# Kernel tuning notes

Hardware: AMD Instinct MI355X
Metric: run time of the kernel (lower is better)

The kernel has to match this reference:

```python
import jax, jax.numpy as jnp
import numpy as np

B, S, K, N, GROUPS, GS = 4, 2048, 4096, 4096, 32, 128


def setup_inputs() -> dict:
    key = jax.random.key(0)
    k1, k2, k3, k4, k5 = jax.random.split(key, 5)
    x = jax.random.normal(k1, (B, S, K), dtype=jnp.float32)
    # int8-stored quantized weights in [-128, 127], layout [K, N] (in_features, out_features)
    weight_int8 = jax.random.randint(k2, (K, N), -128, 128, dtype=jnp.int32)
    # per-group, per-output-column positive scales
    scales = (jax.random.uniform(k3, (GROUPS, N), dtype=jnp.float32) * 0.01 + 1e-4)
    bias = jax.random.normal(k4, (N,), dtype=jnp.float32) * 0.02
    # column reordering permutation (high-sensitivity cols first in the real module)
    col_indices = jax.random.permutation(k5, K).astype(jnp.int32)
    return {"x": x, "scales": scales, "bias": bias,
            "weight_int8": weight_int8, "col_indices": col_indices,
            "group_size": GS}


def reference(x, scales, bias, weight_int8, col_indices, group_size):
    orig_shape = x.shape
    k = x.shape[-1]
    x2 = x.reshape(-1, k)                      # [M, K]
    # CPR column reordering of the activations (weights are stored pre-reordered)
    x_reordered = x2[:, col_indices]           # [M, K]
    # per-group dequant: scale row-group g applies to rows [g*gs, (g+1)*gs) of W
    s_full = jnp.repeat(scales, group_size, axis=0)[:k]          # [K, N]
    w_deq = weight_int8.astype(x.dtype) * s_full                 # [K, N]
    y = x_reordered @ w_deq + bias                               # [M, N]
    return y.reshape(*orig_shape[:-1], y.shape[-1])
```

## Files before the change

kernel.cpp:

```cpp
#include <hip/hip_runtime.h>
#include <hip/hip_bf16.h>

#define M_DIM 8192
#define N_DIM 4096
#define K_DIM 4096
#define NITER 32

typedef __bf16 bf16x8 __attribute__((ext_vector_type(8)));
typedef float f32x4 __attribute__((ext_vector_type(4)));
typedef unsigned short ushort8v __attribute__((ext_vector_type(8)));

typedef const __attribute__((address_space(1))) void gv_t;
typedef __attribute__((address_space(3))) void lv_t;

static __device__ __forceinline__ unsigned short f2bf(float f) {
  unsigned u = __builtin_bit_cast(unsigned, f);
  u += 0x7fffu + ((u >> 16) & 1u);
  return (unsigned short)(u >> 16);
}

__global__ void k_pinv(const int* __restrict__ ci, int* __restrict__ pinv) {
  int k = blockIdx.x * 256 + threadIdx.x;
  if (k < K_DIM) pinv[ci[k]] = k;
}

__global__ void k_cvt(const float* __restrict__ x, unsigned short* __restrict__ xb) {
  const long n4 = (long)M_DIM * K_DIM / 4;
  for (long i = (long)blockIdx.x * 256 + threadIdx.x; i < n4; i += 2048L * 256) {
    float4 v = *(const float4*)(x + i * 4);
    ushort4 o;
    o.x = f2bf(v.x); o.y = f2bf(v.y); o.z = f2bf(v.z); o.w = f2bf(v.w);
    *(ushort4*)(xb + i * 4) = o;
  }
}

__global__ void k_w2t(const int* __restrict__ w, const float* __restrict__ scales,
                      const int* __restrict__ pinv, unsigned short* __restrict__ w2t) {
  __shared__ int tile[64 * 68];
  __shared__ int grp[64];
  __shared__ int krow[64];
  const int n0 = blockIdx.x * 64;
  const int c0 = blockIdx.y * 64;
  const int t = threadIdx.x;
  if (t < 64) {
    int kk = pinv[c0 + t];
    krow[t] = kk;
    grp[t] = kk >> 7;
  }
  __syncthreads();
  {
    const int ci = t >> 2, q = t & 3;
    const int kk = krow[ci];
    const int* src = w + (long)kk * N_DIM + n0 + q * 16;
#pragma unroll
    for (int j = 0; j < 4; ++j) {
      int4 v = *(const int4*)(src + j * 4);
      *(int4*)&tile[ci * 68 + q * 16 + j * 4] = v;
    }
  }
  __syncthreads();
  {
    const int nj = t >> 2, cq = t & 3;
    const int n = n0 + nj;
    unsigned short outv[16];
#pragma unroll
    for (int i = 0; i < 16; ++i) {
      int cii = cq * 16 + i;
      float f = (float)tile[cii * 68 + nj] * scales[grp[cii] * N_DIM + n];
      outv[i] = f2bf(f);
    }
    unsigned short* dst = w2t + (long)n * K_DIM + c0 + cq * 16;
    *(ushort8v*)(dst)     = *(ushort8v*)&outv[0];
    *(ushort8v*)(dst + 8) = *(ushort8v*)&outv[8];
  }
}

#define RD_A4(base) do { const char* _b=(const char*)(base); \
  af[0]=*(const bf16x8*)(_b); af[1]=*(const bf16x8*)(_b+2048); \
  af[2]=*(const bf16x8*)(_b+4096); af[3]=*(const bf16x8*)(_b+6144); } while(0)
#define RD_B4(base) do { const char* _b=(const char*)(base); \
  bf[0]=*(const bf16x8*)(_b); bf[1]=*(const bf16x8*)(_b+2048); \
  bf[2]=*(const bf16x8*)(_b+4096); bf[3]=*(const bf16x8*)(_b+6144); } while(0)
#define MFMA16(o) do { \
  _Pragma("unroll") for (int mi = 0; mi < 4; ++mi) \
  _Pragma("unroll") for (int ni = 0; ni < 4; ++ni) \
    acc[(o)+mi][ni] = __builtin_amdgcn_mfma_f32_16x16x32_bf16(af[mi], bf[ni], acc[(o)+mi][ni], 0, 0, 0); \
  } while(0)
#define GL(s, d) __builtin_amdgcn_global_load_lds((gv_t*)(s), (lv_t*)(d), 16, 0, 0)
#define BAR_IN() do { __builtin_amdgcn_s_barrier(); \
  asm volatile("s_waitcnt lgkmcnt(0)" ::: "memory"); \
  __builtin_amdgcn_sched_barrier(0); } while(0)
#define BAR_OUT() do { __builtin_amdgcn_sched_barrier(0); \
  __builtin_amdgcn_s_barrier(); __builtin_amdgcn_sched_barrier(0); } while(0)
#define VM4() asm volatile("s_waitcnt vmcnt(4)" ::: "memory")

__global__ __launch_bounds__(512, 2) void k_gemm(const unsigned short* __restrict__ A,
                                                 const unsigned short* __restrict__ Bt,
                                                 const float* __restrict__ bias,
                                                 float* __restrict__ C) {
  __shared__ __attribute__((aligned(16))) char lds[131072];
  char* A0 = lds;
  char* B0 = lds + 32768;
  char* A1 = lds + 65536;
  char* B1 = lds + 98304;

  const int bid = blockIdx.x;
  const int swz = (bid & 7) * 64 + (bid >> 3);
  const int by = swz >> 4;
  const int bx = swz & 15;

  const int tid = threadIdx.x;
  const int l = tid & 63;
  const int w = tid >> 6;
  const int wr = w >> 2;
  const int wc = w & 3;
  const int r4 = l & 15;
  const int kb = (l >> 4) << 4;

  const int wmask = ((tid >> 3) & 7) << 4;
  const int kbo = ((tid & 7) * 16) ^ wmask;
  const char* srcA = (const char*)A + (size_t)(by * 256 + (tid >> 3)) * (K_DIM * 2) + kbo;
  const char* srcB = (const char*)Bt + (size_t)(bx * 256 + (tid >> 3)) * (K_DIM * 2) + kbo;
  const int stgoff = tid * 16;

  const int R0A = wr * 128 + r4;
  const int R0B = wc * 64 + r4;
  const int aoff = ((R0A << 7) + kb) ^ ((R0A & 7) << 4);
  const int boff = ((R0B << 7) + kb) ^ ((R0B & 7) << 4);

  f32x4 acc[8][4];
  const f32x4 z = {0.f, 0.f, 0.f, 0.f};
#pragma unroll
  for (int mi = 0; mi < 8; ++mi)
#pragma unroll
    for (int ni = 0; ni < 4; ++ni) acc[mi][ni] = z;

#pragma unroll
  for (int j = 0; j < 4; ++j) GL(srcA + j * 524288, A0 + j * 8192 + stgoff);
#pragma unroll
  for (int j = 0; j < 4; ++j) GL(srcB + j * 524288, B0 + j * 8192 + stgoff);
#pragma unroll
  for (int j = 0; j < 2; ++j) GL(srcB + 128 + j * 524288, B1 + j * 8192 + stgoff);
  asm volatile("s_waitcnt vmcnt(2)" ::: "memory");
  BAR_OUT();

  bf16x8 af[4], bf[4];

  for (int J = 0; J < NITER; ++J) {
    const bool nl = (J < NITER - 1);
    const long ko1 = (long)(2 * J + 1) * 128;
    const long ko2 = ko1 + 128;
    const long ko3 = ko1 + 256;

    RD_A4(A0 + aoff);
    RD_B4(B0 + boff);
    GL(srcB + ko1 + 2 * 524288, B1 + 2 * 8192 + stgoff);
    GL(srcB + ko1 + 3 * 524288, B1 + 3 * 8192 + stgoff);
    BAR_IN();
    __builtin_amdgcn_s_setprio(1); MFMA16(0); __builtin_amdgcn_s_setprio(0);
    VM4();
    BAR_OUT();

    RD_A4(A0 + aoff + 8192);
    GL(srcA + ko1 + 0 * 524288, A1 + 0 * 8192 + stgoff);
    GL(srcA + ko1 + 2 * 524288, A1 + 2 * 8192 + stgoff);
    BAR_IN();
    __builtin_amdgcn_s_setprio(1); MFMA16(4); __builtin_amdgcn_s_setprio(0);
    BAR_OUT();

    RD_A4(A0 + (aoff ^ 64));
    RD_B4(B0 + (boff ^ 64));
    GL(srcA + ko1 + 1 * 524288, A1 + 1 * 8192 + stgoff);
    GL(srcA + ko1 + 3 * 524288, A1 + 3 * 8192 + stgoff);
    BAR_IN();
    __builtin_amdgcn_s_setprio(1); MFMA16(0); __builtin_amdgcn_s_setprio(0);
    BAR_OUT();

    RD_A4(A0 + (aoff ^ 64) + 8192);
    if (nl) {
      GL(srcB + ko2 + 0 * 524288, B0 + 0 * 8192 + stgoff);
      GL(srcB + ko2 + 1 * 524288, B0 + 1 * 8192 + stgoff);
    }
    BAR_IN();
    __builtin_amdgcn_s_setprio(1); MFMA16(4); __builtin_amdgcn_s_setprio(0);
    if (nl) VM4();
    else    asm volatile("s_waitcnt vmcnt(0)" ::: "memory");
    BAR_OUT();

    RD_A4(A1 + aoff);
    RD_B4(B1 + boff);
    if (nl) {
      GL(srcB + ko2 + 2 * 524288, B0 + 2 * 8192 + stgoff);
      GL(srcB + ko2 + 3 * 524288, B0 + 3 * 8192 + stgoff);
    }
    BAR_IN();
    __builtin_amdgcn_s_setprio(1); MFMA16(0); __builtin_amdgcn_s_setprio(0);
    VM4();
    BAR_OUT();

    RD_A4(A1 + aoff + 8192);
    if (nl) {
      GL(srcA + ko2 + 0 * 524288, A0 + 0 * 8192 + stgoff);
      GL(srcA + ko2 + 2 * 524288, A0 + 2 * 8192 + stgoff);
    }
    BAR_IN();
    __builtin_amdgcn_s_setprio(1); MFMA16(4); __builtin_amdgcn_s_setprio(0);
    BAR_OUT();

    RD_A4(A1 + (aoff ^ 64));
    RD_B4(B1 + (boff ^ 64));
    if (nl) {
      GL(srcA + ko2 + 1 * 524288, A0 + 1 * 8192 + stgoff);
      GL(srcA + ko2 + 3 * 524288, A0 + 3 * 8192 + stgoff);
    }
    BAR_IN();
    __builtin_amdgcn_s_setprio(1); MFMA16(0); __builtin_amdgcn_s_setprio(0);
    BAR_OUT();

    RD_A4(A1 + (aoff ^ 64) + 8192);
    if (nl) {
      GL(srcB + ko3 + 0 * 524288, B1 + 0 * 8192 + stgoff);
      GL(srcB + ko3 + 1 * 524288, B1 + 1 * 8192 + stgoff);
    }
    BAR_IN();
    __builtin_amdgcn_s_setprio(1); MFMA16(4); __builtin_amdgcn_s_setprio(0);
    VM4();
    BAR_OUT();
  }

  const int row0 = by * 256 + wr * 128 + ((l >> 4) << 2);
  const int col0 = bx * 256 + wc * 64 + r4;
#pragma unroll
  for (int ni = 0; ni < 4; ++ni) {
    const int col = col0 + ni * 16;
    const float bv = bias[col];
#pragma unroll
    for (int mi = 0; mi < 8; ++mi) {
#pragma unroll
      for (int r = 0; r < 4; ++r)
        C[(size_t)(row0 + mi * 16 + r) * N_DIM + col] = acc[mi][ni][r] + bv;
    }
  }
}

__global__ void k_fallback(const float* __restrict__ x, const float* __restrict__ scales,
                           const float* __restrict__ bias, const int* __restrict__ w,
                           const int* __restrict__ ci, float* __restrict__ out) {
  const int n = blockIdx.x * 256 + threadIdx.x;
  const int m0 = blockIdx.y * 32;
  float acc[32];
#pragma unroll
  for (int i = 0; i < 32; ++i) acc[i] = 0.f;
  for (int k = 0; k < K_DIM; ++k) {
    int c = ci[k];
    float wv = (float)w[(long)k * N_DIM + n] * scales[(k >> 7) * N_DIM + n];
#pragma unroll 8
    for (int mm = 0; mm < 32; ++mm)
      acc[mm] += x[(long)(m0 + mm) * K_DIM + c] * wv;
  }
  float bv = bias[n];
  for (int mm = 0; mm < 32; ++mm)
    out[(long)(m0 + mm) * N_DIM + n] = acc[mm] + bv;
}

extern "C" void kernel_launch(void* const* d_in, const int* in_sizes, int n_in,
                              void* d_out, int out_size, void* d_ws, size_t ws_size,
                              hipStream_t stream) {
  const float* x      = (const float*)d_in[0];
  const float* scales = (const float*)d_in[1];
  const float* bias   = (const float*)d_in[2];
  const int*   wq     = (const int*)d_in[3];
  const int*   ci     = (const int*)d_in[4];
  float* out = (float*)d_out;

  const size_t xb_bytes  = (size_t)M_DIM * K_DIM * 2;
  const size_t w2t_bytes = (size_t)N_DIM * K_DIM * 2;
  const size_t need = xb_bytes + w2t_bytes + (size_t)K_DIM * 4;

  if (ws_size < need) {
    k_fallback<<<dim3(N_DIM / 256, M_DIM / 32), 256, 0, stream>>>(x, scales, bias, wq, ci, out);
    return;
  }

  unsigned short* xb  = (unsigned short*)d_ws;
  unsigned short* w2t = (unsigned short*)((char*)d_ws + xb_bytes);
  int* pinv           = (int*)((char*)d_ws + xb_bytes + w2t_bytes);

  k_pinv<<<K_DIM / 256, 256, 0, stream>>>(ci, pinv);
  k_cvt<<<2048, 256, 0, stream>>>(x, xb);
  k_w2t<<<dim3(N_DIM / 64, K_DIM / 64), 256, 0, stream>>>(wq, scales, pinv, w2t);
  k_gemm<<<(M_DIM / 256) * (N_DIM / 256), 512, 0, stream>>>(xb, w2t, bias, out);
}
```

Measured before the change: 298.8 us.

## Switch GEMM inner loop from 16x16x32 to 32x32x16 bf16 MFMA tiles

Replaces the per-wave 8x4 grid of 16x16x32 MFMAs with a 4x2 grid of 32x32x16 MFMAs over the same 128x64 warp tile. LDS read addressing, the swizzle and the output epilogue row mapping are reworked to match the 32x32 accumulator layout. The intent is fewer MFMA issues and fewer LDS fragment reads per flop. The vmcnt waits are also renumbered to fit the new load count. The risk is accumulator register pressure and new LDS bank-conflict patterns from the changed swizzle.

New measurement: 323.5 us. 1.08x slower.

```diff
diff --git a/kernel.cpp b/kernel.cpp
--- a/kernel.cpp
+++ b/kernel.cpp
@@ -7,7 +7,7 @@
 #define NITER 32
 
 typedef __bf16 bf16x8 __attribute__((ext_vector_type(8)));
-typedef float f32x4 __attribute__((ext_vector_type(4)));
+typedef float f32x16 __attribute__((ext_vector_type(16)));
 typedef unsigned short ushort8v __attribute__((ext_vector_type(8)));
 
 typedef const __attribute__((address_space(1))) void gv_t;
@@ -75,16 +75,25 @@
   }
 }
 
-#define RD_A4(base) do { const char* _b=(const char*)(base); \
-  af[0]=*(const bf16x8*)(_b); af[1]=*(const bf16x8*)(_b+2048); \
-  af[2]=*(const bf16x8*)(_b+4096); af[3]=*(const bf16x8*)(_b+6144); } while(0)
-#define RD_B4(base) do { const char* _b=(const char*)(base); \
-  bf[0]=*(const bf16x8*)(_b); bf[1]=*(const bf16x8*)(_b+2048); \
-  bf[2]=*(const bf16x8*)(_b+4096); bf[3]=*(const bf16x8*)(_b+6144); } while(0)
-#define MFMA16(o) do { \
-  _Pragma("unroll") for (int mi = 0; mi < 4; ++mi) \
-  _Pragma("unroll") for (int ni = 0; ni < 4; ++ni) \
-    acc[(o)+mi][ni] = __builtin_amdgcn_mfma_f32_16x16x32_bf16(af[mi], bf[ni], acc[(o)+mi][ni], 0, 0, 0); \
+#define RDA(mh, bo, jp) do { \
+  af[0][0]=*(const bf16x8*)(lds+(bo)+(vA0^(((2*(jp))    )<<5))+((mh)*2+0)*4096); \
+  af[0][1]=*(const bf16x8*)(lds+(bo)+(vA0^(((2*(jp))+1  )<<5))+((mh)*2+0)*4096); \
+  af[1][0]=*(const bf16x8*)(lds+(bo)+(vA0^(((2*(jp))    )<<5))+((mh)*2+1)*4096); \
+  af[1][1]=*(const bf16x8*)(lds+(bo)+(vA0^(((2*(jp))+1  )<<5))+((mh)*2+1)*4096); } while(0)
+#define RDB(bo, jp) do { \
+  bf[0][0]=*(const bf16x8*)(lds+(bo)+32768+(vB0^(((2*(jp))  )<<5))      ); \
+  bf[0][1]=*(const bf16x8*)(lds+(bo)+32768+(vB0^(((2*(jp))+1)<<5))      ); \
+  bf[1][0]=*(const bf16x8*)(lds+(bo)+32768+(vB0^(((2*(jp))  )<<5))+4096 ); \
+  bf[1][1]=*(const bf16x8*)(lds+(bo)+32768+(vB0^(((2*(jp))+1)<<5))+4096 ); } while(0)
+#define MFMA8(mh) do { \
+  acc[(mh)*2+0][0]=__builtin_amdgcn_mfma_f32_32x32x16_bf16(af[0][0],bf[0][0],acc[(mh)*2+0][0],0,0,0); \
+  acc[(mh)*2+0][1]=__builtin_amdgcn_mfma_f32_32x32x16_bf16(af[0][0],bf[1][0],acc[(mh)*2+0][1],0,0,0); \
+  acc[(mh)*2+1][0]=__builtin_amdgcn_mfma_f32_32x32x16_bf16(af[1][0],bf[0][0],acc[(mh)*2+1][0],0,0,0); \
+  acc[(mh)*2+1][1]=__builtin_amdgcn_mfma_f32_32x32x16_bf16(af[1][0],bf[1][0],acc[(mh)*2+1][1],0,0,0); \
+  acc[(mh)*2+0][0]=__builtin_amdgcn_mfma_f32_32x32x16_bf16(af[0][1],bf[0][1],acc[(mh)*2+0][0],0,0,0); \
+  acc[(mh)*2+0][1]=__builtin_amdgcn_mfma_f32_32x32x16_bf16(af[0][1],bf[1][1],acc[(mh)*2+0][1],0,0,0); \
+  acc[(mh)*2+1][0]=__builtin_amdgcn_mfma_f32_32x32x16_bf16(af[1][1],bf[0][1],acc[(mh)*2+1][0],0,0,0); \
+  acc[(mh)*2+1][1]=__builtin_amdgcn_mfma_f32_32x32x16_bf16(af[1][1],bf[1][1],acc[(mh)*2+1][1],0,0,0); \
   } while(0)
 #define GL(s, d) __builtin_amdgcn_global_load_lds((gv_t*)(s), (lv_t*)(d), 16, 0, 0)
 #define BAR_IN() do { __builtin_amdgcn_s_barrier(); \
@@ -92,17 +101,12 @@
   __builtin_amdgcn_sched_barrier(0); } while(0)
 #define BAR_OUT() do { __builtin_amdgcn_sched_barrier(0); \
   __builtin_amdgcn_s_barrier(); __builtin_amdgcn_sched_barrier(0); } while(0)
-#define VM4() asm volatile("s_waitcnt vmcnt(4)" ::: "memory")
 
 __global__ __launch_bounds__(512, 2) void k_gemm(const unsigned short* __restrict__ A,
                                                  const unsigned short* __restrict__ Bt,
                                                  const float* __restrict__ bias,
                                                  float* __restrict__ C) {
   __shared__ __attribute__((aligned(16))) char lds[131072];
-  char* A0 = lds;
-  char* B0 = lds + 32768;
-  char* A1 = lds + 65536;
-  char* B1 = lds + 98304;
 
   const int bid = blockIdx.x;
   const int swz = (bid & 7) * 64 + (bid >> 3);
@@ -114,8 +118,6 @@
   const int w = tid >> 6;
   const int wr = w >> 2;
   const int wc = w & 3;
-  const int r4 = l & 15;
-  const int kb = (l >> 4) << 4;
 
   const int wmask = ((tid >> 3) & 7) << 4;
   const int kbo = ((tid & 7) * 16) ^ wmask;
@@ -123,28 +125,32 @@
   const char* srcB = (const char*)Bt + (size_t)(bx * 256 + (tid >> 3)) * (K_DIM * 2) + kbo;
   const int stgoff = tid * 16;
 
-  const int R0A = wr * 128 + r4;
-  const int R0B = wc * 64 + r4;
-  const int aoff = ((R0A << 7) + kb) ^ ((R0A & 7) << 4);
-  const int boff = ((R0B << 7) + kb) ^ ((R0B & 7) << 4);
-
-  f32x4 acc[8][4];
-  const f32x4 z = {0.f, 0.f, 0.f, 0.f};
-#pragma unroll
-  for (int mi = 0; mi < 8; ++mi)
-#pragma unroll
-    for (int ni = 0; ni < 4; ++ni) acc[mi][ni] = z;
-
-#pragma unroll
-  for (int j = 0; j < 4; ++j) GL(srcA + j * 524288, A0 + j * 8192 + stgoff);
-#pragma unroll
-  for (int j = 0; j < 4; ++j) GL(srcB + j * 524288, B0 + j * 8192 + stgoff);
-#pragma unroll
-  for (int j = 0; j < 2; ++j) GL(srcB + 128 + j * 524288, B1 + j * 8192 + stgoff);
+  const int lane31 = l & 31;
+  const int klo = (l >> 5) << 4;
+  const int rA = wr * 128 + lane31;
+  const int rB = wc * 64 + lane31;
+  const int mk = (l & 7) << 4;
+  const int vA0 = ((rA << 7) | klo) ^ mk;
+  const int vB0 = ((rB << 7) | klo) ^ mk;
+
+  f32x16 acc[4][2];
+#pragma unroll
+  for (int mi = 0; mi < 4; ++mi)
+#pragma unroll
+    for (int ni = 0; ni < 2; ++ni)
+#pragma unroll
+      for (int r = 0; r < 16; ++r) acc[mi][ni][r] = 0.f;
+
+#pragma unroll
+  for (int j = 0; j < 4; ++j) GL(srcA + j * 524288, lds + j * 8192 + stgoff);
+#pragma unroll
+  for (int j = 0; j < 4; ++j) GL(srcB + j * 524288, lds + 32768 + j * 8192 + stgoff);
+#pragma unroll
+  for (int j = 0; j < 2; ++j) GL(srcB + 128 + j * 524288, lds + 98304 + j * 8192 + stgoff);
   asm volatile("s_waitcnt vmcnt(2)" ::: "memory");
   BAR_OUT();
 
-  bf16x8 af[4], bf[4];
+  bf16x8 af[2][2], bf[2][2];
 
   for (int J = 0; J < NITER; ++J) {
     const bool nl = (J < NITER - 1);
@@ -152,93 +158,89 @@
     const long ko2 = ko1 + 128;
     const long ko3 = ko1 + 256;
 
-    RD_A4(A0 + aoff);
-    RD_B4(B0 + boff);
-    GL(srcB + ko1 + 2 * 524288, B1 + 2 * 8192 + stgoff);
-    GL(srcB + ko1 + 3 * 524288, B1 + 3 * 8192 + stgoff);
-    BAR_IN();
-    __builtin_amdgcn_s_setprio(1); MFMA16(0); __builtin_amdgcn_s_setprio(0);
-    VM4();
-    BAR_OUT();
-
-    RD_A4(A0 + aoff + 8192);
-    GL(srcA + ko1 + 0 * 524288, A1 + 0 * 8192 + stgoff);
-    GL(srcA + ko1 + 2 * 524288, A1 + 2 * 8192 + stgoff);
-    BAR_IN();
-    __builtin_amdgcn_s_setprio(1); MFMA16(4); __builtin_amdgcn_s_setprio(0);
-    BAR_OUT();
-
-    RD_A4(A0 + (aoff ^ 64));
-    RD_B4(B0 + (boff ^ 64));
-    GL(srcA + ko1 + 1 * 524288, A1 + 1 * 8192 + stgoff);
-    GL(srcA + ko1 + 3 * 524288, A1 + 3 * 8192 + stgoff);
-    BAR_IN();
-    __builtin_amdgcn_s_setprio(1); MFMA16(0); __builtin_amdgcn_s_setprio(0);
-    BAR_OUT();
-
-    RD_A4(A0 + (aoff ^ 64) + 8192);
-    if (nl) {
-      GL(srcB + ko2 + 0 * 524288, B0 + 0 * 8192 + stgoff);
-      GL(srcB + ko2 + 1 * 524288, B0 + 1 * 8192 + stgoff);
-    }
-    BAR_IN();
-    __builtin_amdgcn_s_setprio(1); MFMA16(4); __builtin_amdgcn_s_setprio(0);
-    if (nl) VM4();
+    RDA(0, 0, 0); RDB(0, 0);
+    GL(srcB + ko1 + 2 * 524288, lds + 98304 + 2 * 8192 + stgoff);
+    GL(srcB + ko1 + 3 * 524288, lds + 98304 + 3 * 8192 + stgoff);
+    BAR_IN();
+    __builtin_amdgcn_s_setprio(1); MFMA8(0); __builtin_amdgcn_s_setprio(0);
+    BAR_OUT();
+
+    RDA(1, 0, 0);
+    GL(srcA + ko1 + 0 * 524288, lds + 65536 + 0 * 8192 + stgoff);
+    GL(srcA + ko1 + 2 * 524288, lds + 65536 + 2 * 8192 + stgoff);
+    BAR_IN();
+    __builtin_amdgcn_s_setprio(1); MFMA8(1); __builtin_amdgcn_s_setprio(0);
+    BAR_OUT();
+
+    RDA(0, 0, 1); RDB(0, 1);
+    GL(srcA + ko1 + 1 * 524288, lds + 65536 + 1 * 8192 + stgoff);
+    GL(srcA + ko1 + 3 * 524288, lds + 65536 + 3 * 8192 + stgoff);
+    BAR_IN();
+    __builtin_amdgcn_s_setprio(1); MFMA8(0); __builtin_amdgcn_s_setprio(0);
+    BAR_OUT();
+
+    RDA(1, 0, 1);
+    if (nl) {
+      GL(srcB + ko2 + 0 * 524288, lds + 32768 + 0 * 8192 + stgoff);
+      GL(srcB + ko2 + 1 * 524288, lds + 32768 + 1 * 8192 + stgoff);
+    }
+    BAR_IN();
+    __builtin_amdgcn_s_setprio(1); MFMA8(1); __builtin_amdgcn_s_setprio(0);
+    if (nl) asm volatile("s_waitcnt vmcnt(2)" ::: "memory");
     else    asm volatile("s_waitcnt vmcnt(0)" ::: "memory");
     BAR_OUT();
 
-    RD_A4(A1 + aoff);
-    RD_B4(B1 + boff);
-    if (nl) {
-      GL(srcB + ko2 + 2 * 524288, B0 + 2 * 8192 + stgoff);
-      GL(srcB + ko2 + 3 * 524288, B0 + 3 * 8192 + stgoff);
-    }
-    BAR_IN();
-    __builtin_amdgcn_s_setprio(1); MFMA16(0); __builtin_amdgcn_s_setprio(0);
-    VM4();
-    BAR_OUT();
-
-    RD_A4(A1 + aoff + 8192);
-    if (nl) {
-      GL(srcA + ko2 + 0 * 524288, A0 + 0 * 8192 + stgoff);
-      GL(srcA + ko2 + 2 * 524288, A0 + 2 * 8192 + stgoff);
-    }
-    BAR_IN();
-    __builtin_amdgcn_s_setprio(1); MFMA16(4); __builtin_amdgcn_s_setprio(0);
-    BAR_OUT();
-
-    RD_A4(A1 + (aoff ^ 64));
-    RD_B4(B1 + (boff ^ 64));
-    if (nl) {
-      GL(srcA + ko2 + 1 * 524288, A0 + 1 * 8192 + stgoff);
-      GL(srcA + ko2 + 3 * 524288, A0 + 3 * 8192 + stgoff);
-    }
-    BAR_IN();
-    __builtin_amdgcn_s_setprio(1); MFMA16(0); __builtin_amdgcn_s_setprio(0);
-    BAR_OUT();
-
-    RD_A4(A1 + (aoff ^ 64) + 8192);
-    if (nl) {
-      GL(srcB + ko3 + 0 * 524288, B1 + 0 * 8192 + stgoff);
-      GL(srcB + ko3 + 1 * 524288, B1 + 1 * 8192 + stgoff);
-    }
-    BAR_IN();
-    __builtin_amdgcn_s_setprio(1); MFMA16(4); __builtin_amdgcn_s_setprio(0);
-    VM4();
-    BAR_OUT();
-  }
-
-  const int row0 = by * 256 + wr * 128 + ((l >> 4) << 2);
-  const int col0 = bx * 256 + wc * 64 + r4;
-#pragma unroll
-  for (int ni = 0; ni < 4; ++ni) {
-    const int col = col0 + ni * 16;
+    RDA(0, 65536, 0); RDB(65536, 0);
+    if (nl) {
+      GL(srcB + ko2 + 2 * 524288, lds + 32768 + 2 * 8192 + stgoff);
+      GL(srcB + ko2 + 3 * 524288, lds + 32768 + 3 * 8192 + stgoff);
+    }
+    BAR_IN();
+    __builtin_amdgcn_s_setprio(1); MFMA8(0); __builtin_amdgcn_s_setprio(0);
+    BAR_OUT();
+
+    RDA(1, 65536, 0);
+    if (nl) {
+      GL(srcA + ko2 + 0 * 524288, lds + 0 * 8192 + stgoff);
+      GL(srcA + ko2 + 2 * 524288, lds + 2 * 8192 + stgoff);
+    }
+    BAR_IN();
+    __builtin_amdgcn_s_setprio(1); MFMA8(1); __builtin_amdgcn_s_setprio(0);
+    BAR_OUT();
+
+    RDA(0, 65536, 1); RDB(65536, 1);
+    if (nl) {
+      GL(srcA + ko2 + 1 * 524288, lds + 1 * 8192 + stgoff);
+      GL(srcA + ko2 + 3 * 524288, lds + 3 * 8192 + stgoff);
+    }
+    BAR_IN();
+    __builtin_amdgcn_s_setprio(1); MFMA8(0); __builtin_amdgcn_s_setprio(0);
+    BAR_OUT();
+
+    RDA(1, 65536, 1);
+    if (nl) {
+      GL(srcB + ko3 + 0 * 524288, lds + 98304 + 0 * 8192 + stgoff);
+      GL(srcB + ko3 + 1 * 524288, lds + 98304 + 1 * 8192 + stgoff);
+    }
+    BAR_IN();
+    __builtin_amdgcn_s_setprio(1); MFMA8(1); __builtin_amdgcn_s_setprio(0);
+    asm volatile("s_waitcnt vmcnt(2)" ::: "memory");
+    BAR_OUT();
+  }
+
+  const int row0 = by * 256 + wr * 128 + ((l >> 5) << 2);
+  const int col0 = bx * 256 + wc * 64 + lane31;
+#pragma unroll
+  for (int ni = 0; ni < 2; ++ni) {
+    const int col = col0 + ni * 32;
     const float bv = bias[col];
 #pragma unroll
-    for (int mi = 0; mi < 8; ++mi) {
-#pragma unroll
-      for (int r = 0; r < 4; ++r)
-        C[(size_t)(row0 + mi * 16 + r) * N_DIM + col] = acc[mi][ni][r] + bv;
+    for (int mi = 0; mi < 4; ++mi) {
+#pragma unroll
+      for (int r = 0; r < 16; ++r) {
+        const int row = row0 + mi * 32 + (r & 3) + ((r >> 2) << 3);
+        C[(size_t)row * N_DIM + col] = acc[mi][ni][r] + bv;
+      }
     }
   }
 }
```

## Double-buffer MFMA fragments in registers and overlap LDS reads with compute

Applied to the files above, without the earlier changes.

Splits the A/B fragment registers into even/odd sets so the LDS reads for the next MFMA phase are issued before the current phase's MFMAs. Each phase then waits only on partial lgkmcnt (4 or 8 outstanding) instead of draining all LDS reads. The vmcnt waits are restructured from VM4 to VM2 at different points. This hides LDS latency behind matrix math, at the cost of extra VGPRs under the 512x2 launch bound and more delicate wait-count correctness.

Result: no change. 303.4 us (+1.5%).

```diff
diff --git a/kernel.cpp b/kernel.cpp
--- a/kernel.cpp
+++ b/kernel.cpp
@@ -75,24 +75,28 @@
   }
 }
 
-#define RD_A4(base) do { const char* _b=(const char*)(base); \
-  af[0]=*(const bf16x8*)(_b); af[1]=*(const bf16x8*)(_b+2048); \
-  af[2]=*(const bf16x8*)(_b+4096); af[3]=*(const bf16x8*)(_b+6144); } while(0)
-#define RD_B4(base) do { const char* _b=(const char*)(base); \
-  bf[0]=*(const bf16x8*)(_b); bf[1]=*(const bf16x8*)(_b+2048); \
-  bf[2]=*(const bf16x8*)(_b+4096); bf[3]=*(const bf16x8*)(_b+6144); } while(0)
-#define MFMA16(o) do { \
+#define RD4(dst, base) do { const char* _b=(const char*)(base); \
+  dst[0]=*(const bf16x8*)(_b); dst[1]=*(const bf16x8*)(_b+2048); \
+  dst[2]=*(const bf16x8*)(_b+4096); dst[3]=*(const bf16x8*)(_b+6144); } while(0)
+#define MFMA16(AF, BF, o) do { \
   _Pragma("unroll") for (int mi = 0; mi < 4; ++mi) \
   _Pragma("unroll") for (int ni = 0; ni < 4; ++ni) \
-    acc[(o)+mi][ni] = __builtin_amdgcn_mfma_f32_16x16x32_bf16(af[mi], bf[ni], acc[(o)+mi][ni], 0, 0, 0); \
+    acc[(o)+mi][ni] = __builtin_amdgcn_mfma_f32_16x16x32_bf16(AF[mi], BF[ni], acc[(o)+mi][ni], 0, 0, 0); \
   } while(0)
 #define GL(s, d) __builtin_amdgcn_global_load_lds((gv_t*)(s), (lv_t*)(d), 16, 0, 0)
-#define BAR_IN() do { __builtin_amdgcn_s_barrier(); \
+#define BAR_L0() do { __builtin_amdgcn_s_barrier(); \
   asm volatile("s_waitcnt lgkmcnt(0)" ::: "memory"); \
+  __builtin_amdgcn_sched_barrier(0); } while(0)
+#define BAR_L4() do { __builtin_amdgcn_s_barrier(); \
+  asm volatile("s_waitcnt lgkmcnt(4)" ::: "memory"); \
+  __builtin_amdgcn_sched_barrier(0); } while(0)
+#define BAR_L8() do { __builtin_amdgcn_s_barrier(); \
+  asm volatile("s_waitcnt lgkmcnt(8)" ::: "memory"); \
   __builtin_amdgcn_sched_barrier(0); } while(0)
 #define BAR_OUT() do { __builtin_amdgcn_sched_barrier(0); \
   __builtin_amdgcn_s_barrier(); __builtin_amdgcn_sched_barrier(0); } while(0)
-#define VM4() asm volatile("s_waitcnt vmcnt(4)" ::: "memory")
+#define VM2() do { asm volatile("s_waitcnt vmcnt(2)" ::: "memory"); \
+  __builtin_amdgcn_sched_barrier(0); } while(0)
 
 __global__ __launch_bounds__(512, 2) void k_gemm(const unsigned short* __restrict__ A,
                                                  const unsigned short* __restrict__ Bt,
@@ -144,7 +148,7 @@
   asm volatile("s_waitcnt vmcnt(2)" ::: "memory");
   BAR_OUT();
 
-  bf16x8 af[4], bf[4];
+  bf16x8 af_e[4], af_o[4], bf_e[4], bf_o[4];
 
   for (int J = 0; J < NITER; ++J) {
     const bool nl = (J < NITER - 1);
@@ -152,79 +156,77 @@
     const long ko2 = ko1 + 128;
     const long ko3 = ko1 + 256;
 
-    RD_A4(A0 + aoff);
-    RD_B4(B0 + boff);
+    RD4(af_e, A0 + aoff);
+    RD4(bf_e, B0 + boff);
+    RD4(af_o, A0 + aoff + 8192);
     GL(srcB + ko1 + 2 * 524288, B1 + 2 * 8192 + stgoff);
     GL(srcB + ko1 + 3 * 524288, B1 + 3 * 8192 + stgoff);
-    BAR_IN();
-    __builtin_amdgcn_s_setprio(1); MFMA16(0); __builtin_amdgcn_s_setprio(0);
-    VM4();
-    BAR_OUT();
-
-    RD_A4(A0 + aoff + 8192);
+    BAR_L4();
+    __builtin_amdgcn_s_setprio(1); MFMA16(af_e, bf_e, 0); __builtin_amdgcn_s_setprio(0);
+    BAR_OUT();
+
+    RD4(af_e, A0 + (aoff ^ 64));
+    RD4(bf_o, B0 + (boff ^ 64));
     GL(srcA + ko1 + 0 * 524288, A1 + 0 * 8192 + stgoff);
     GL(srcA + ko1 + 2 * 524288, A1 + 2 * 8192 + stgoff);
-    BAR_IN();
-    __builtin_amdgcn_s_setprio(1); MFMA16(4); __builtin_amdgcn_s_setprio(0);
-    BAR_OUT();
-
-    RD_A4(A0 + (aoff ^ 64));
-    RD_B4(B0 + (boff ^ 64));
+    BAR_L8();
+    __builtin_amdgcn_s_setprio(1); MFMA16(af_o, bf_e, 4); __builtin_amdgcn_s_setprio(0);
+    BAR_OUT();
+
+    RD4(af_o, A0 + (aoff ^ 64) + 8192);
     GL(srcA + ko1 + 1 * 524288, A1 + 1 * 8192 + stgoff);
     GL(srcA + ko1 + 3 * 524288, A1 + 3 * 8192 + stgoff);
-    BAR_IN();
-    __builtin_amdgcn_s_setprio(1); MFMA16(0); __builtin_amdgcn_s_setprio(0);
-    BAR_OUT();
-
-    RD_A4(A0 + (aoff ^ 64) + 8192);
+    BAR_L4();
+    __builtin_amdgcn_s_setprio(1); MFMA16(af_e, bf_o, 0); __builtin_amdgcn_s_setprio(0);
+    BAR_OUT();
+
     if (nl) {
       GL(srcB + ko2 + 0 * 524288, B0 + 0 * 8192 + stgoff);
       GL(srcB + ko2 + 1 * 524288, B0 + 1 * 8192 + stgoff);
     }
-    BAR_IN();
-    __builtin_amdgcn_s_setprio(1); MFMA16(4); __builtin_amdgcn_s_setprio(0);
-    if (nl) VM4();
-    else    asm volatile("s_waitcnt vmcnt(0)" ::: "memory");
-    BAR_OUT();
-
-    RD_A4(A1 + aoff);
-    RD_B4(B1 + boff);
+    BAR_L0();
+    __builtin_amdgcn_s_setprio(1); MFMA16(af_o, bf_o, 4); __builtin_amdgcn_s_setprio(0);
+    if (nl) VM2();
+    else { asm volatile("s_waitcnt vmcnt(0)" ::: "memory"); __builtin_amdgcn_sched_barrier(0); }
+    BAR_OUT();
+
+    RD4(af_e, A1 + aoff);
+    RD4(bf_e, B1 + boff);
+    RD4(af_o, A1 + aoff + 8192);
     if (nl) {
       GL(srcB + ko2 + 2 * 524288, B0 + 2 * 8192 + stgoff);
       GL(srcB + ko2 + 3 * 524288, B0 + 3 * 8192 + stgoff);
     }
-    BAR_IN();
-    __builtin_amdgcn_s_setprio(1); MFMA16(0); __builtin_amdgcn_s_setprio(0);
-    VM4();
-    BAR_OUT();
-
-    RD_A4(A1 + aoff + 8192);
+    BAR_L4();
+    __builtin_amdgcn_s_setprio(1); MFMA16(af_e, bf_e, 0); __builtin_amdgcn_s_setprio(0);
+    BAR_OUT();
+
+    RD4(af_e, A1 + (aoff ^ 64));
+    RD4(bf_o, B1 + (boff ^ 64));
     if (nl) {
       GL(srcA + ko2 + 0 * 524288, A0 + 0 * 8192 + stgoff);
       GL(srcA + ko2 + 2 * 524288, A0 + 2 * 8192 + stgoff);
     }
-    BAR_IN();
-    __builtin_amdgcn_s_setprio(1); MFMA16(4); __builtin_amdgcn_s_setprio(0);
-    BAR_OUT();
-
-    RD_A4(A1 + (aoff ^ 64));
-    RD_B4(B1 + (boff ^ 64));
+    BAR_L8();
+    __builtin_amdgcn_s_setprio(1); MFMA16(af_o, bf_e, 4); __builtin_amdgcn_s_setprio(0);
+    BAR_OUT();
+
+    RD4(af_o, A1 + (aoff ^ 64) + 8192);
     if (nl) {
       GL(srcA + ko2 + 1 * 524288, A0 + 1 * 8192 + stgoff);
       GL(srcA + ko2 + 3 * 524288, A0 + 3 * 8192 + stgoff);
     }
-    BAR_IN();
-    __builtin_amdgcn_s_setprio(1); MFMA16(0); __builtin_amdgcn_s_setprio(0);
-    BAR_OUT();
-
-    RD_A4(A1 + (aoff ^ 64) + 8192);
+    BAR_L4();
+    __builtin_amdgcn_s_setprio(1); MFMA16(af_e, bf_o, 0); __builtin_amdgcn_s_setprio(0);
+    BAR_OUT();
+
     if (nl) {
       GL(srcB + ko3 + 0 * 524288, B1 + 0 * 8192 + stgoff);
       GL(srcB + ko3 + 1 * 524288, B1 + 1 * 8192 + stgoff);
     }
-    BAR_IN();
-    __builtin_amdgcn_s_setprio(1); MFMA16(4); __builtin_amdgcn_s_setprio(0);
-    VM4();
+    BAR_L0();
+    __builtin_amdgcn_s_setprio(1); MFMA16(af_o, bf_o, 4); __builtin_amdgcn_s_setprio(0);
+    VM2();
     BAR_OUT();
   }
 
```
